# Performance work log

Measured on AMD Instinct MI355X. Metric: run time of the kernel, lower is better.

## Reference

```python
import jax, jax.numpy as jnp
import numpy as np

N, BOND, PHYS = 784, 4, 2
BS = 16384
STD = 1e-08


def setup_inputs() -> dict:
    key = jax.random.key(0)
    k1, k2 = jax.random.split(key)
    data = jax.random.randint(k1, (BS, N), 0, 2).astype(jnp.float32)
    bias = jnp.eye(BOND, dtype=jnp.float32)[:, :, None].repeat(PHYS, axis=2)  # (BOND,BOND,PHYS)
    tensors = STD * jax.random.normal(k2, (N, BOND, BOND, PHYS), dtype=jnp.float32) + bias
    return {"data": data, "tensors": tensors}


def reference(data, tensors):
    # data: (bs, n) in {0,1}; tensors: (n, D, D, P)
    bs, n = data.shape
    emb = jnp.stack([data, 1.0 - data], axis=2)  # (bs, n, P)
    # per-site transfer matrices for every sample: (n, bs, D, D)
    mats = jnp.einsum('nlri,bni->nblr', tensors, emb)
    left0 = mats[0][:, 0, :]  # (bs, D)  -- row 0 of site-0 matrix
    lx0 = jax.nn.log_softmax(tensors[0, 0, 0])  # (P,)

    def step(left, xs):
        t, m = xs  # t: (D, D, P), m: (bs, D, D)
        logits = left @ t[:, 0, :]              # (bs, P)
        lx = jax.nn.log_softmax(logits, axis=1)  # (bs, P)
        new_left = jnp.einsum('bl,blr->br', left, m)
        return new_left, lx

    _, lxs = jax.lax.scan(step, left0, (tensors[1:], mats[1:]))  # (n-1, bs, P)
    logx = jnp.concatenate(
        [jnp.broadcast_to(lx0, (1, bs, PHYS)), lxs], axis=0)  # (n, bs, P)
    logx = jnp.transpose(logx, (1, 0, 2))  # (bs, n, P)
    log_prob = logx[..., 0] * data + logx[..., 1] * (1.0 - data)
    return log_prob.sum(-1)  # (bs,)
```

## Files before the change

kernel.cpp:

```cpp
#include <hip/hip_runtime.h>

#define NSITES 784
#define BS_TOT 16384
#define K_SEG 28
#define G_SEG 28

#define STEP(sbit, TP) do {                                                          \
    const float* t_ = (TP);                                                          \
    float p00 = fmaf(left0, t_[0],  fmaf(left1, t_[8],  fmaf(left2, t_[16], left3 * t_[24]))); \
    float p01 = fmaf(left0, t_[1],  fmaf(left1, t_[9],  fmaf(left2, t_[17], left3 * t_[25]))); \
    float p10 = fmaf(left0, t_[2],  fmaf(left1, t_[10], fmaf(left2, t_[18], left3 * t_[26]))); \
    float p11 = fmaf(left0, t_[3],  fmaf(left1, t_[11], fmaf(left2, t_[19], left3 * t_[27]))); \
    float p20 = fmaf(left0, t_[4],  fmaf(left1, t_[12], fmaf(left2, t_[20], left3 * t_[28]))); \
    float p21 = fmaf(left0, t_[5],  fmaf(left1, t_[13], fmaf(left2, t_[21], left3 * t_[29]))); \
    float p30 = fmaf(left0, t_[6],  fmaf(left1, t_[14], fmaf(left2, t_[22], left3 * t_[30]))); \
    float p31 = fmaf(left0, t_[7],  fmaf(left1, t_[15], fmaf(left2, t_[23], left3 * t_[31]))); \
    bool s_ = (sbit);                                                                \
    float lg0 = p00, lg1 = p01;                                                      \
    float mx_ = fmaxf(lg0, lg1);                                                     \
    float ch_ = s_ ? lg0 : lg1;                                                      \
    acc_nat += (ch_ - mx_);                                                          \
    float ad_ = fabsf(lg0 - lg1);                                                    \
    acc_l2 += __builtin_amdgcn_logf(1.0f + __builtin_amdgcn_exp2f(-ad_ * 1.4426950408889634f)); \
    left0 = s_ ? p00 : p01;                                                          \
    left1 = s_ ? p10 : p11;                                                          \
    left2 = s_ ? p20 : p21;                                                          \
    left3 = s_ ? p30 : p31;                                                          \
} while (0)

#define MM_ROW(Q, Pr) do {                                                           \
    Q.x = fmaf(Pr.x, m0.x, fmaf(Pr.y, m1.x, fmaf(Pr.z, m2.x, Pr.w * m3.x)));         \
    Q.y = fmaf(Pr.x, m0.y, fmaf(Pr.y, m1.y, fmaf(Pr.z, m2.y, Pr.w * m3.y)));         \
    Q.z = fmaf(Pr.x, m0.z, fmaf(Pr.y, m1.z, fmaf(Pr.z, m2.z, Pr.w * m3.z)));         \
    Q.w = fmaf(Pr.x, m0.w, fmaf(Pr.y, m1.w, fmaf(Pr.z, m2.w, Pr.w * m3.w)));         \
} while (0)

__global__ __launch_bounds__(256) void pack_kernel(const float* __restrict__ data,
                                                   unsigned long long* __restrict__ packed) {
    int gid  = blockIdx.x * 256 + threadIdx.x;
    int row  = gid >> 6;
    int lane = threadIdx.x & 63;
    const float* r = data + (size_t)row * NSITES;
    #pragma unroll
    for (int w = 0; w < 12; ++w) {
        unsigned long long m = __ballot(r[w * 64 + lane] == 1.0f);
        if (lane == 0) packed[(size_t)w * BS_TOT + row] = m;
    }
    float v = (lane < 16) ? r[768 + lane] : 0.0f;
    unsigned long long m = __ballot((lane < 16) && (v == 1.0f));
    if (lane == 0) packed[(size_t)12 * BS_TOT + row] = m;
}

__device__ __forceinline__ unsigned long long bit_window(
        const unsigned long long* __restrict__ packed, int n0, int b) {
    int a0 = n0 >> 6, s = n0 & 63;
    unsigned long long w0 = packed[(size_t)a0 * BS_TOT + b];
    unsigned long long w1 = packed[(size_t)(a0 + 1) * BS_TOT + b];
    return s ? ((w0 >> s) | (w1 << (64 - s))) : w0;
}

__global__ __launch_bounds__(256) void phase1_kernel(const float* __restrict__ tensors,
                                                     const unsigned long long* __restrict__ packed,
                                                     float* __restrict__ Pbuf) {
    int b = blockIdx.x * 256 + threadIdx.x;
    int k = blockIdx.y;

    __shared__ __align__(16) float lt[G_SEG * 32];
    const float* g = tensors + (size_t)k * G_SEG * 32;
    for (int e = threadIdx.x; e < G_SEG * 32; e += 256) {
        int i = e >> 5, rem = e & 31;
        int l = rem >> 3, r = (rem >> 1) & 3, p = rem & 1;
        lt[i * 32 + p * 16 + l * 4 + r] = g[e];
    }
    __syncthreads();

    unsigned long long win = bit_window(packed, k * G_SEG, b);

    const float4* ms = (const float4*)&lt[(win & 1ull) ? 0 : 16];
    float4 P0 = ms[0], P1 = ms[1], P2 = ms[2], P3 = ms[3];

    #pragma unroll 3
    for (int i = 1; i < G_SEG; ++i) {
        const float4* mi = (const float4*)&lt[i * 32 + (((win >> i) & 1ull) ? 0 : 16)];
        float4 m0 = mi[0], m1 = mi[1], m2 = mi[2], m3 = mi[3];
        float4 Q0, Q1, Q2, Q3;
        MM_ROW(Q0, P0); MM_ROW(Q1, P1); MM_ROW(Q2, P2); MM_ROW(Q3, P3);
        P0 = Q0; P1 = Q1; P2 = Q2; P3 = Q3;
    }

    float4* pb = (float4*)(Pbuf + ((size_t)k * BS_TOT + b) * 16);
    pb[0] = P0; pb[1] = P1; pb[2] = P2; pb[3] = P3;
}

__global__ __launch_bounds__(64) void phase2_kernel(const float* __restrict__ Pbuf,
                                                    float* __restrict__ prefix) {
    int b = blockIdx.x * 64 + threadIdx.x;
    float l0 = 1.0f, l1 = 0.0f, l2 = 0.0f, l3 = 0.0f;
    const float4* base = (const float4*)Pbuf + (size_t)b * 4;
    #pragma unroll
    for (int k = 0; k < K_SEG; ++k) {
        prefix[((size_t)k * 4 + 0) * BS_TOT + b] = l0;
        prefix[((size_t)k * 4 + 1) * BS_TOT + b] = l1;
        prefix[((size_t)k * 4 + 2) * BS_TOT + b] = l2;
        prefix[((size_t)k * 4 + 3) * BS_TOT + b] = l3;
        if (k == K_SEG - 1) break;
        const float4* pb = base + (size_t)k * BS_TOT * 4;
        float4 r0 = pb[0], r1 = pb[1], r2 = pb[2], r3 = pb[3];
        float n0 = fmaf(l0, r0.x, fmaf(l1, r1.x, fmaf(l2, r2.x, l3 * r3.x)));
        float n1 = fmaf(l0, r0.y, fmaf(l1, r1.y, fmaf(l2, r2.y, l3 * r3.y)));
        float n2 = fmaf(l0, r0.z, fmaf(l1, r1.z, fmaf(l2, r2.z, l3 * r3.z)));
        float n3 = fmaf(l0, r0.w, fmaf(l1, r1.w, fmaf(l2, r2.w, l3 * r3.w)));
        l0 = n0; l1 = n1; l2 = n2; l3 = n3;
    }
}

__global__ __launch_bounds__(256) void phase3_kernel(const float* __restrict__ tensors,
                                                     const unsigned long long* __restrict__ packed,
                                                     const float* __restrict__ prefix,
                                                     float* __restrict__ res) {
    int b = blockIdx.x * 256 + threadIdx.x;
    int k = blockIdx.y;
    const float* tb = tensors + (size_t)k * G_SEG * 32;

    float left0 = prefix[((size_t)k * 4 + 0) * BS_TOT + b];
    float left1 = prefix[((size_t)k * 4 + 1) * BS_TOT + b];
    float left2 = prefix[((size_t)k * 4 + 2) * BS_TOT + b];
    float left3 = prefix[((size_t)k * 4 + 3) * BS_TOT + b];
    float acc_nat = 0.0f, acc_l2 = 0.0f;

    unsigned long long win = bit_window(packed, k * G_SEG, b);
    #pragma unroll 4
    for (int i = 0; i < G_SEG; ++i) {
        STEP(((win >> i) & 1ull) != 0, tb + i * 32);
    }
    res[(size_t)k * BS_TOT + b] = acc_nat - 0.6931471805599453f * acc_l2;
}

__global__ __launch_bounds__(256) void reduce_kernel(const float* __restrict__ res,
                                                     float* __restrict__ out) {
    int b = blockIdx.x * 256 + threadIdx.x;
    float a = 0.0f;
    #pragma unroll
    for (int k = 0; k < K_SEG; ++k) a += res[(size_t)k * BS_TOT + b];
    out[b] = a;
}

__global__ __launch_bounds__(64) void amps_chain_kernel(
    const float* __restrict__ data, const float* __restrict__ tensors,
    float* __restrict__ out)
{
    int b = blockIdx.x * blockDim.x + threadIdx.x;
    if (b >= BS_TOT) return;
    const float* row = data + (size_t)b * NSITES;
    float left0 = 1.0f, left1 = 0.0f, left2 = 0.0f, left3 = 0.0f;
    float acc_nat = 0.0f, acc_l2 = 0.0f;
    for (int n = 0; n < NSITES; ++n) {
        STEP(row[n] == 1.0f, tensors + (size_t)n * 32);
    }
    out[b] = acc_nat - 0.6931471805599453f * acc_l2;
}

extern "C" void kernel_launch(void* const* d_in, const int* in_sizes, int n_in,
                              void* d_out, int out_size, void* d_ws, size_t ws_size,
                              hipStream_t stream) {
    const float* data    = (const float*)d_in[0];
    const float* tensors = (const float*)d_in[1];
    float* out = (float*)d_out;

    const size_t packed_bytes = (size_t)13 * BS_TOT * 8;
    const size_t Pbuf_bytes   = (size_t)K_SEG * BS_TOT * 16 * 4;
    const size_t prefix_bytes = (size_t)K_SEG * 4 * BS_TOT * 4;
    const size_t res_bytes    = (size_t)K_SEG * BS_TOT * 4;
    const size_t need = packed_bytes + Pbuf_bytes + prefix_bytes + res_bytes;

    if (ws_size < need) {
        hipLaunchKernelGGL(amps_chain_kernel, dim3(BS_TOT / 64), dim3(64), 0, stream,
                           data, tensors, out);
        return;
    }

    char* wsb = (char*)d_ws;
    unsigned long long* packed = (unsigned long long*)wsb;
    float* Pbuf   = (float*)(wsb + packed_bytes);
    float* prefix = (float*)(wsb + packed_bytes + Pbuf_bytes);
    float* res    = (float*)(wsb + packed_bytes + Pbuf_bytes + prefix_bytes);

    hipLaunchKernelGGL(pack_kernel,   dim3((BS_TOT * 64) / 256), dim3(256), 0, stream,
                       data, packed);
    hipLaunchKernelGGL(phase1_kernel, dim3(BS_TOT / 256, K_SEG - 1), dim3(256), 0, stream,
                       tensors, packed, Pbuf);
    hipLaunchKernelGGL(phase2_kernel, dim3(BS_TOT / 64), dim3(64), 0, stream, Pbuf, prefix);
    hipLaunchKernelGGL(phase3_kernel, dim3(BS_TOT / 256, K_SEG), dim3(256), 0, stream,
                       tensors, packed, prefix, res);
    hipLaunchKernelGGL(reduce_kernel, dim3(BS_TOT / 256), dim3(256), 0, stream, res, out);
}
```

Baseline: 64.88 us.

## Fuse prefix scan, segment walk and reduction into one kernel with shared memory

Merges phase2 (cross-segment prefix scan), phase3 (per-segment log-prob walk) and the final reduction into a single kernel. Prefixes and per-segment results now live in shared memory instead of global buffers. The segment count changes from 28x28 to 16x49, so phase1 writes fewer partial products. This removes two launches and the global prefix and result round trips. In exchange, one wave serially computes the prefix while the other seven waves wait, and each thread walks longer 49-step segments, which lowers parallelism.

```diff
diff --git a/kernel.cpp b/kernel.cpp
--- a/kernel.cpp
+++ b/kernel.cpp
@@ -2,8 +2,9 @@
 
 #define NSITES 784
 #define BS_TOT 16384
-#define K_SEG 28
-#define G_SEG 28
+#define KSEG 16
+#define GSEG 49
+#define WPB  64
 
 #define STEP(sbit, TP) do {                                                          \
     const float* t_ = (TP);                                                          \
@@ -16,11 +17,10 @@
     float p30 = fmaf(left0, t_[6],  fmaf(left1, t_[14], fmaf(left2, t_[22], left3 * t_[30]))); \
     float p31 = fmaf(left0, t_[7],  fmaf(left1, t_[15], fmaf(left2, t_[23], left3 * t_[31]))); \
     bool s_ = (sbit);                                                                \
-    float lg0 = p00, lg1 = p01;                                                      \
-    float mx_ = fmaxf(lg0, lg1);                                                     \
-    float ch_ = s_ ? lg0 : lg1;                                                      \
+    float mx_ = fmaxf(p00, p01);                                                     \
+    float ch_ = s_ ? p00 : p01;                                                      \
     acc_nat += (ch_ - mx_);                                                          \
-    float ad_ = fabsf(lg0 - lg1);                                                    \
+    float ad_ = fabsf(p00 - p01);                                                    \
     acc_l2 += __builtin_amdgcn_logf(1.0f + __builtin_amdgcn_exp2f(-ad_ * 1.4426950408889634f)); \
     left0 = s_ ? p00 : p01;                                                          \
     left1 = s_ ? p10 : p11;                                                          \
@@ -65,22 +65,22 @@
     int b = blockIdx.x * 256 + threadIdx.x;
     int k = blockIdx.y;
 
-    __shared__ __align__(16) float lt[G_SEG * 32];
-    const float* g = tensors + (size_t)k * G_SEG * 32;
-    for (int e = threadIdx.x; e < G_SEG * 32; e += 256) {
+    __shared__ __align__(16) float lt[GSEG * 32];
+    const float* g = tensors + (size_t)k * GSEG * 32;
+    for (int e = threadIdx.x; e < GSEG * 32; e += 256) {
         int i = e >> 5, rem = e & 31;
         int l = rem >> 3, r = (rem >> 1) & 3, p = rem & 1;
         lt[i * 32 + p * 16 + l * 4 + r] = g[e];
     }
     __syncthreads();
 
-    unsigned long long win = bit_window(packed, k * G_SEG, b);
+    unsigned long long win = bit_window(packed, k * GSEG, b);
 
     const float4* ms = (const float4*)&lt[(win & 1ull) ? 0 : 16];
     float4 P0 = ms[0], P1 = ms[1], P2 = ms[2], P3 = ms[3];
 
     #pragma unroll 3
-    for (int i = 1; i < G_SEG; ++i) {
+    for (int i = 1; i < GSEG; ++i) {
         const float4* mi = (const float4*)&lt[i * 32 + (((win >> i) & 1ull) ? 0 : 16)];
         float4 m0 = mi[0], m1 = mi[1], m2 = mi[2], m3 = mi[3];
         float4 Q0, Q1, Q2, Q3;
@@ -92,57 +92,65 @@
     pb[0] = P0; pb[1] = P1; pb[2] = P2; pb[3] = P3;
 }
 
-__global__ __launch_bounds__(64) void phase2_kernel(const float* __restrict__ Pbuf,
-                                                    float* __restrict__ prefix) {
-    int b = blockIdx.x * 64 + threadIdx.x;
-    float l0 = 1.0f, l1 = 0.0f, l2 = 0.0f, l3 = 0.0f;
-    const float4* base = (const float4*)Pbuf + (size_t)b * 4;
+__global__ __launch_bounds__(512, 8) void scan_walk_kernel(
+    const float* __restrict__ tensors,
+    const unsigned long long* __restrict__ packed,
+    const float* __restrict__ Pbuf,
+    float* __restrict__ out)
+{
+    __shared__ float sPre[KSEG][4][WPB];
+    __shared__ float sRes[KSEG][WPB];
+
+    const int t    = threadIdx.x;
+    const int wv   = t >> 6;
+    const int lane = t & 63;
+    const int s0   = blockIdx.x * WPB;
+    const int b    = s0 + lane;
+
+    if (wv == 0) {
+        float l0 = 1.0f, l1 = 0.0f, l2 = 0.0f, l3 = 0.0f;
+        const float4* base = (const float4*)Pbuf + (size_t)b * 4;
+        #pragma unroll
+        for (int k = 0; k < KSEG; ++k) {
+            sPre[k][0][lane] = l0; sPre[k][1][lane] = l1;
+            sPre[k][2][lane] = l2; sPre[k][3][lane] = l3;
+            if (k < KSEG - 1) {
+                const float4* pb = base + (size_t)k * BS_TOT * 4;
+                float4 r0 = pb[0], r1 = pb[1], r2 = pb[2], r3 = pb[3];
+                float n0 = fmaf(l0, r0.x, fmaf(l1, r1.x, fmaf(l2, r2.x, l3 * r3.x)));
+                float n1 = fmaf(l0, r0.y, fmaf(l1, r1.y, fmaf(l2, r2.y, l3 * r3.y)));
+                float n2 = fmaf(l0, r0.z, fmaf(l1, r1.z, fmaf(l2, r2.z, l3 * r3.z)));
+                float n3 = fmaf(l0, r0.w, fmaf(l1, r1.w, fmaf(l2, r2.w, l3 * r3.w)));
+                l0 = n0; l1 = n1; l2 = n2; l3 = n3;
+            }
+        }
+    }
+    __syncthreads();
+
     #pragma unroll
-    for (int k = 0; k < K_SEG; ++k) {
-        prefix[((size_t)k * 4 + 0) * BS_TOT + b] = l0;
-        prefix[((size_t)k * 4 + 1) * BS_TOT + b] = l1;
-        prefix[((size_t)k * 4 + 2) * BS_TOT + b] = l2;
-        prefix[((size_t)k * 4 + 3) * BS_TOT + b] = l3;
-        if (k == K_SEG - 1) break;
-        const float4* pb = base + (size_t)k * BS_TOT * 4;
-        float4 r0 = pb[0], r1 = pb[1], r2 = pb[2], r3 = pb[3];
-        float n0 = fmaf(l0, r0.x, fmaf(l1, r1.x, fmaf(l2, r2.x, l3 * r3.x)));
-        float n1 = fmaf(l0, r0.y, fmaf(l1, r1.y, fmaf(l2, r2.y, l3 * r3.y)));
-        float n2 = fmaf(l0, r0.z, fmaf(l1, r1.z, fmaf(l2, r2.z, l3 * r3.z)));
-        float n3 = fmaf(l0, r0.w, fmaf(l1, r1.w, fmaf(l2, r2.w, l3 * r3.w)));
-        l0 = n0; l1 = n1; l2 = n2; l3 = n3;
+    for (int rep = 0; rep < 2; ++rep) {
+        const int k  = wv + rep * 8;
+        const int n0 = k * GSEG;
+        const float* tb = tensors + (size_t)n0 * 32;
+        unsigned long long win = bit_window(packed, n0, b);
+
+        float left0 = sPre[k][0][lane], left1 = sPre[k][1][lane];
+        float left2 = sPre[k][2][lane], left3 = sPre[k][3][lane];
+        float acc_nat = 0.0f, acc_l2 = 0.0f;
+        #pragma unroll 7
+        for (int i = 0; i < GSEG; ++i) {
+            STEP(((win >> i) & 1ull) != 0, tb + i * 32);
+        }
+        sRes[k][lane] = acc_nat - 0.6931471805599453f * acc_l2;
     }
-}
+    __syncthreads();
 
-__global__ __launch_bounds__(256) void phase3_kernel(const float* __restrict__ tensors,
-                                                     const unsigned long long* __restrict__ packed,
-                                                     const float* __restrict__ prefix,
-                                                     float* __restrict__ res) {
-    int b = blockIdx.x * 256 + threadIdx.x;
-    int k = blockIdx.y;
-    const float* tb = tensors + (size_t)k * G_SEG * 32;
-
-    float left0 = prefix[((size_t)k * 4 + 0) * BS_TOT + b];
-    float left1 = prefix[((size_t)k * 4 + 1) * BS_TOT + b];
-    float left2 = prefix[((size_t)k * 4 + 2) * BS_TOT + b];
-    float left3 = prefix[((size_t)k * 4 + 3) * BS_TOT + b];
-    float acc_nat = 0.0f, acc_l2 = 0.0f;
-
-    unsigned long long win = bit_window(packed, k * G_SEG, b);
-    #pragma unroll 4
-    for (int i = 0; i < G_SEG; ++i) {
-        STEP(((win >> i) & 1ull) != 0, tb + i * 32);
+    if (wv == 0) {
+        float acc = 0.0f;
+        #pragma unroll
+        for (int kk = 0; kk < KSEG; ++kk) acc += sRes[kk][lane];
+        out[b] = acc;
     }
-    res[(size_t)k * BS_TOT + b] = acc_nat - 0.6931471805599453f * acc_l2;
-}
-
-__global__ __launch_bounds__(256) void reduce_kernel(const float* __restrict__ res,
-                                                     float* __restrict__ out) {
-    int b = blockIdx.x * 256 + threadIdx.x;
-    float a = 0.0f;
-    #pragma unroll
-    for (int k = 0; k < K_SEG; ++k) a += res[(size_t)k * BS_TOT + b];
-    out[b] = a;
 }
 
 __global__ __launch_bounds__(64) void amps_chain_kernel(
@@ -168,10 +176,8 @@
     float* out = (float*)d_out;
 
     const size_t packed_bytes = (size_t)13 * BS_TOT * 8;
-    const size_t Pbuf_bytes   = (size_t)K_SEG * BS_TOT * 16 * 4;
-    const size_t prefix_bytes = (size_t)K_SEG * 4 * BS_TOT * 4;
-    const size_t res_bytes    = (size_t)K_SEG * BS_TOT * 4;
-    const size_t need = packed_bytes + Pbuf_bytes + prefix_bytes + res_bytes;
+    const size_t Pbuf_bytes   = (size_t)(KSEG - 1) * BS_TOT * 16 * 4;
+    const size_t need = packed_bytes + Pbuf_bytes;
 
     if (ws_size < need) {
         hipLaunchKernelGGL(amps_chain_kernel, dim3(BS_TOT / 64), dim3(64), 0, stream,
@@ -181,16 +187,12 @@
 
     char* wsb = (char*)d_ws;
     unsigned long long* packed = (unsigned long long*)wsb;
-    float* Pbuf   = (float*)(wsb + packed_bytes);
-    float* prefix = (float*)(wsb + packed_bytes + Pbuf_bytes);
-    float* res    = (float*)(wsb + packed_bytes + Pbuf_bytes + prefix_bytes);
+    float* Pbuf = (float*)(wsb + packed_bytes);
 
-    hipLaunchKernelGGL(pack_kernel,   dim3((BS_TOT * 64) / 256), dim3(256), 0, stream,
+    hipLaunchKernelGGL(pack_kernel,      dim3((BS_TOT * 64) / 256), dim3(256), 0, stream,
                        data, packed);
-    hipLaunchKernelGGL(phase1_kernel, dim3(BS_TOT / 256, K_SEG - 1), dim3(256), 0, stream,
+    hipLaunchKernelGGL(phase1_kernel,    dim3(BS_TOT / 256, KSEG - 1), dim3(256), 0, stream,
                        tensors, packed, Pbuf);
-    hipLaunchKernelGGL(phase2_kernel, dim3(BS_TOT / 64), dim3(64), 0, stream, Pbuf, prefix);
-    hipLaunchKernelGGL(phase3_kernel, dim3(BS_TOT / 256, K_SEG), dim3(256), 0, stream,
-                       tensors, packed, prefix, res);
-    hipLaunchKernelGGL(reduce_kernel, dim3(BS_TOT / 256), dim3(256), 0, stream, res, out);
+    hipLaunchKernelGGL(scan_walk_kernel, dim3(BS_TOT / WPB), dim3(512), 0, stream,
+                       tensors, packed, Pbuf, out);
 }
```

Measured after the change: 89.76 us. 1.38x slower.
